# Performance work log

Measured on AMD Instinct MI355X. Metric: run time of the kernel, lower is better.

Reference implementation:

```python
import jax, jax.numpy as jnp
import numpy as np

B, N, D_IN, D_H, D_OUT = 32, 512, 512, 512, 512


def _xavier(key, fan_in, fan_out):
    bound = np.sqrt(6.0 / (fan_in + fan_out))
    return jax.random.uniform(key, (fan_in, fan_out), jnp.float32, -bound, bound)


def setup_inputs() -> dict:
    key = jax.random.key(0)
    ks = jax.random.split(key, 8)
    batch_graph = jax.random.normal(ks[0], (B, N, D_IN), jnp.float32)
    adj = jax.random.uniform(ks[1], (B, N, N), jnp.float32)  # per-graph adjacency blocks
    W0 = _xavier(ks[2], D_IN, D_H)
    b0 = jnp.zeros((D_H,), jnp.float32)
    W1 = _xavier(ks[3], D_H, D_H)
    b1 = jnp.zeros((D_H,), jnp.float32)
    W2 = _xavier(ks[4], D_H, D_OUT)
    b2 = jnp.zeros((D_OUT,), jnp.float32)
    return {"batch_graph": batch_graph, "adj": adj,
            "W0": W0, "b0": b0, "W1": W1, "b1": b1, "W2": W2, "b2": b2}


def _gcn_layer(h, adj, W, b):
    # GraphConvolution: adj @ (h @ W) + b, batched per graph.
    # Equivalent to big_adj @ (big_graph @ W) since big_adj is block-diagonal.
    support = jnp.einsum('bnd,de->bne', h, W)
    return jnp.einsum('bnm,bme->bne', adj, support) + b


def reference(batch_graph, adj, W0, b0, W1, b1, W2, b2):
    # dropout is identity at inference time
    h = jax.nn.relu(_gcn_layer(batch_graph, adj, W0, b0))
    h = jax.nn.relu(_gcn_layer(h, adj, W1, b1))
    h = _gcn_layer(h, adj, W2, b2)  # no activation on final layer
    return h  # [B, N, D_OUT] == torch.stack(big_graph.split(N))
```

## Files before the change

### kernel.cpp

```cpp
#include <hip/hip_runtime.h>
#include <stdint.h>

typedef __bf16 bf16x8 __attribute__((ext_vector_type(8)));
typedef float f32x4 __attribute__((ext_vector_type(4)));
typedef unsigned short u16x4 __attribute__((ext_vector_type(4)));

static __device__ __forceinline__ unsigned short f2bf(float f) {
    union { float f; unsigned u; } v; v.f = f;
    unsigned r = (v.u + 0x7FFFu + ((v.u >> 16) & 1u)) >> 16;
    return (unsigned short)r;
}

__global__ void prep_kernel(const float* __restrict__ X,
                            const float* __restrict__ adj,
                            const float* __restrict__ W0,
                            const float* __restrict__ W1,
                            const float* __restrict__ W2,
                            unsigned short* __restrict__ bufH,
                            unsigned short* __restrict__ adjB,
                            unsigned short* __restrict__ Wt) {
    const int bid = blockIdx.x;
    const int t = threadIdx.x;
    if (bid < 16384) {
        const float* src = (bid < 8192) ? X : adj;
        unsigned short* dst = (bid < 8192) ? bufH : adjB;
        const int i = (bid & 8191) * 256 + t;
        f32x4 v = ((const f32x4*)src)[i];
        u16x4 o;
        o.x = f2bf(v.x); o.y = f2bf(v.y); o.z = f2bf(v.z); o.w = f2bf(v.w);
        ((u16x4*)dst)[i] = o;
    } else {
        const int wb = bid - 16384;
        const int z = wb >> 8;
        const int tile = wb & 255;
        const float* W = (z == 0) ? W0 : (z == 1) ? W1 : W2;
        unsigned short* out = Wt + (size_t)z * (512 * 512);
        __shared__ float tileS[32][33];
        const int bx = (tile & 15) * 32, by = (tile >> 4) * 32;
        const int tx = t & 31, ty = t >> 5;
        #pragma unroll
        for (int r = 0; r < 32; r += 8)
            tileS[ty + r][tx] = W[(size_t)(by + ty + r) * 512 + (bx + tx)];
        __syncthreads();
        #pragma unroll
        for (int r = 0; r < 32; r += 8)
            out[(size_t)(bx + ty + r) * 512 + (by + tx)] = f2bf(tileS[tx][ty + r]);
    }
}

template<int LDA, int LDB, int LDO, bool BIAS, bool RELU, typename OT>
__global__ __launch_bounds__(256, 4)
void gemm_abT_ct(const unsigned short* __restrict__ A,
                 const unsigned short* __restrict__ B,
                 OT* __restrict__ out, const float* __restrict__ bias,
                 long batchA, long batchB, long batchO) {
    __shared__ unsigned short As[128 * 64];
    __shared__ unsigned short Bs[64 * 64];

    const int tid  = threadIdx.x;
    const int lane = tid & 63;
    const int wave = tid >> 6;
    const int quad = lane >> 4;
    const int l16  = lane & 15;
    const int wm   = wave & 1;
    const int wn   = wave >> 1;

    const int m0 = blockIdx.x * 128;
    const int n0 = blockIdx.y * 64;
    A   += (size_t)blockIdx.z * batchA;
    B   += (size_t)blockIdx.z * batchB;
    out += (size_t)blockIdx.z * batchO;

    const int srow = tid >> 3;
    const int spos = (tid & 7) ^ (srow & 7);
    const unsigned short* aG = A + (size_t)(m0 + srow) * LDA + spos * 8;
    const unsigned short* bG = B + (size_t)(n0 + srow) * LDB + spos * 8;
    char* aL = (char*)As + tid * 16;
    char* bL = (char*)Bs + tid * 16;

    f32x4 acc[4][2];
    #pragma unroll
    for (int i = 0; i < 4; ++i)
        #pragma unroll
        for (int j = 0; j < 2; ++j) {
            f32x4 z = {0.f, 0.f, 0.f, 0.f};
            acc[i][j] = z;
        }

    #pragma unroll 1
    for (int kk = 0; kk < 8; ++kk) {
        const int ko = kk * 64;
        #pragma unroll
        for (int r = 0; r < 4; ++r) {
            __builtin_amdgcn_global_load_lds(
                (__attribute__((address_space(1))) void*)(uintptr_t)(aG + (size_t)(r * 32) * LDA + ko),
                (__attribute__((address_space(3))) void*)(aL + r * 4096), 16, 0, 0);
        }
        #pragma unroll
        for (int r = 0; r < 2; ++r) {
            __builtin_amdgcn_global_load_lds(
                (__attribute__((address_space(1))) void*)(uintptr_t)(bG + (size_t)(r * 32) * LDB + ko),
                (__attribute__((address_space(3))) void*)(bL + r * 4096), 16, 0, 0);
        }
        __syncthreads();

        #pragma unroll
        for (int ks = 0; ks < 2; ++ks) {
            bf16x8 af[4], bfr[2];
            #pragma unroll
            for (int i = 0; i < 4; ++i) {
                const int row = wm * 64 + i * 16 + l16;
                const int idx = row * 8 + ((ks * 4 + quad) ^ (row & 7));
                af[i] = *(const bf16x8*)((const char*)As + idx * 16);
            }
            #pragma unroll
            for (int j = 0; j < 2; ++j) {
                const int row = wn * 32 + j * 16 + l16;
                const int idx = row * 8 + ((ks * 4 + quad) ^ (row & 7));
                bfr[j] = *(const bf16x8*)((const char*)Bs + idx * 16);
            }
            #pragma unroll
            for (int i = 0; i < 4; ++i)
                #pragma unroll
                for (int j = 0; j < 2; ++j)
                    acc[i][j] = __builtin_amdgcn_mfma_f32_16x16x32_bf16(af[i], bfr[j], acc[i][j], 0, 0, 0);
        }
        __syncthreads();
    }

    #pragma unroll
    for (int i = 0; i < 4; ++i) {
        const int mb = m0 + wm * 64 + i * 16 + quad * 4;
        f32x4 bb = {0.f, 0.f, 0.f, 0.f};
        if constexpr (BIAS) bb = *(const f32x4*)(bias + mb);
        #pragma unroll
        for (int j = 0; j < 2; ++j) {
            const int n = n0 + wn * 32 + j * 16 + l16;
            f32x4 v = acc[i][j];
            if constexpr (BIAS) v += bb;
            if constexpr (RELU) {
                v.x = v.x > 0.f ? v.x : 0.f;
                v.y = v.y > 0.f ? v.y : 0.f;
                v.z = v.z > 0.f ? v.z : 0.f;
                v.w = v.w > 0.f ? v.w : 0.f;
            }
            if constexpr (sizeof(OT) == 4) {
                *(f32x4*)((float*)out + (size_t)n * LDO + mb) = v;
            } else {
                u16x4 o;
                o.x = f2bf(v.x); o.y = f2bf(v.y); o.z = f2bf(v.z); o.w = f2bf(v.w);
                *(u16x4*)((unsigned short*)out + (size_t)n * LDO + mb) = o;
            }
        }
    }
}

extern "C" void kernel_launch(void* const* d_in, const int* in_sizes, int n_in,
                              void* d_out, int out_size, void* d_ws, size_t ws_size,
                              hipStream_t stream) {
    (void)in_sizes; (void)n_in; (void)out_size; (void)ws_size;
    const float* X   = (const float*)d_in[0];
    const float* adj = (const float*)d_in[1];
    const float* W0  = (const float*)d_in[2];
    const float* b0  = (const float*)d_in[3];
    const float* W1  = (const float*)d_in[4];
    const float* b1  = (const float*)d_in[5];
    const float* W2  = (const float*)d_in[6];
    const float* b2  = (const float*)d_in[7];
    float* out = (float*)d_out;

    char* ws = (char*)d_ws;
    const size_t SZ = 16777216;
    unsigned short* adjB = (unsigned short*)(ws);
    unsigned short* bufH = (unsigned short*)(ws + SZ);
    unsigned short* tmpT = (unsigned short*)(ws + 2 * SZ);
    unsigned short* Wt   = (unsigned short*)(ws + 3 * SZ);
    const unsigned short* W0t = Wt;
    const unsigned short* W1t = Wt + 262144;
    const unsigned short* W2t = Wt + 2 * 262144;

    prep_kernel<<<16384 + 768, 256, 0, stream>>>(X, adj, W0, W1, W2, bufH, adjB, Wt);

    const long BATCH = 512L * 512L;

    gemm_abT_ct<512, 512, 16384, false, false, unsigned short>
        <<<dim3(128, 8, 1), 256, 0, stream>>>(bufH, W0t, tmpT, nullptr, 0, 0, 0);
    gemm_abT_ct<16384, 512, 512, true, true, unsigned short>
        <<<dim3(4, 8, 32), 256, 0, stream>>>(tmpT, adjB, bufH, b0, 512, BATCH, BATCH);
    gemm_abT_ct<512, 512, 16384, false, false, unsigned short>
        <<<dim3(128, 8, 1), 256, 0, stream>>>(bufH, W1t, tmpT, nullptr, 0, 0, 0);
    gemm_abT_ct<16384, 512, 512, true, true, unsigned short>
        <<<dim3(4, 8, 32), 256, 0, stream>>>(tmpT, adjB, bufH, b1, 512, BATCH, BATCH);
    gemm_abT_ct<512, 512, 16384, false, false, unsigned short>
        <<<dim3(128, 8, 1), 256, 0, stream>>>(bufH, W2t, tmpT, nullptr, 0, 0, 0);
    gemm_abT_ct<16384, 512, 512, true, false, float>
        <<<dim3(4, 8, 32), 256, 0, stream>>>(tmpT, adjB, out, b2, 512, BATCH, BATCH);
}
```

Before: 228.5 us.

## Fuse prep and all six GEMMs into one cooperative persistent kernel

Replaces seven separate launches with a single cooperative kernel of 512 blocks that converts inputs, transposes the weights, and runs all six GEMM phases, separated by grid-wide syncs. Each block processes two tiles per phase. The aim is to remove per-launch overhead and tail gaps between kernels. In exchange, occupancy is capped at 2 blocks per CU with fixed tile assignment, grid.sync adds its own cost, and the multi-launch path is kept as a fallback if the cooperative launch fails.

```diff
diff --git a/kernel.cpp b/kernel.cpp
--- a/kernel.cpp
+++ b/kernel.cpp
@@ -1,5 +1,8 @@
 #include <hip/hip_runtime.h>
+#include <hip/hip_cooperative_groups.h>
 #include <stdint.h>
+
+namespace cg = cooperative_groups;
 
 typedef __bf16 bf16x8 __attribute__((ext_vector_type(8)));
 typedef float f32x4 __attribute__((ext_vector_type(4)));
@@ -9,6 +12,208 @@
     union { float f; unsigned u; } v; v.f = f;
     unsigned r = (v.u + 0x7FFFu + ((v.u >> 16) & 1u)) >> 16;
     return (unsigned short)r;
+}
+
+template<bool BIAS, bool RELU, typename OT>
+__device__ __forceinline__
+void gemm_tile(const unsigned short* __restrict__ A, int LDA,
+               const unsigned short* __restrict__ B, int LDB,
+               OT* __restrict__ out, int LDO,
+               const float* __restrict__ bias,
+               int m0, int n0,
+               unsigned short* As, unsigned short* Bs) {
+    const int tid  = threadIdx.x;
+    const int lane = tid & 63;
+    const int wave = tid >> 6;
+    const int quad = lane >> 4;
+    const int l16  = lane & 15;
+    const int wm   = wave & 1;
+    const int wn   = wave >> 1;
+
+    const int srow = tid >> 3;
+    const int spos = (tid & 7) ^ (srow & 7);
+    const unsigned short* aG = A + (size_t)(m0 + srow) * LDA + spos * 8;
+    const unsigned short* bG = B + (size_t)(n0 + srow) * LDB + spos * 8;
+    char* aL = (char*)As + tid * 16;
+    char* bL = (char*)Bs + tid * 16;
+
+    f32x4 acc[4][2];
+    #pragma unroll
+    for (int i = 0; i < 4; ++i)
+        #pragma unroll
+        for (int j = 0; j < 2; ++j) {
+            f32x4 z = {0.f, 0.f, 0.f, 0.f};
+            acc[i][j] = z;
+        }
+
+    #pragma unroll 1
+    for (int kk = 0; kk < 8; ++kk) {
+        const int ko = kk * 64;
+        #pragma unroll
+        for (int r = 0; r < 4; ++r)
+            __builtin_amdgcn_global_load_lds(
+                (__attribute__((address_space(1))) void*)(uintptr_t)(aG + (size_t)(r * 32) * LDA + ko),
+                (__attribute__((address_space(3))) void*)(aL + r * 4096), 16, 0, 0);
+        #pragma unroll
+        for (int r = 0; r < 2; ++r)
+            __builtin_amdgcn_global_load_lds(
+                (__attribute__((address_space(1))) void*)(uintptr_t)(bG + (size_t)(r * 32) * LDB + ko),
+                (__attribute__((address_space(3))) void*)(bL + r * 4096), 16, 0, 0);
+        __syncthreads();
+
+        #pragma unroll
+        for (int ks = 0; ks < 2; ++ks) {
+            bf16x8 af[4], bfr[2];
+            #pragma unroll
+            for (int i = 0; i < 4; ++i) {
+                const int row = wm * 64 + i * 16 + l16;
+                const int idx = row * 8 + ((ks * 4 + quad) ^ (row & 7));
+                af[i] = *(const bf16x8*)((const char*)As + idx * 16);
+            }
+            #pragma unroll
+            for (int j = 0; j < 2; ++j) {
+                const int row = wn * 32 + j * 16 + l16;
+                const int idx = row * 8 + ((ks * 4 + quad) ^ (row & 7));
+                bfr[j] = *(const bf16x8*)((const char*)Bs + idx * 16);
+            }
+            #pragma unroll
+            for (int i = 0; i < 4; ++i)
+                #pragma unroll
+                for (int j = 0; j < 2; ++j)
+                    acc[i][j] = __builtin_amdgcn_mfma_f32_16x16x32_bf16(af[i], bfr[j], acc[i][j], 0, 0, 0);
+        }
+        __syncthreads();
+    }
+
+    #pragma unroll
+    for (int i = 0; i < 4; ++i) {
+        const int mb = m0 + wm * 64 + i * 16 + quad * 4;
+        f32x4 bb = {0.f, 0.f, 0.f, 0.f};
+        if constexpr (BIAS) bb = *(const f32x4*)(bias + (mb - m0) + m0);
+        #pragma unroll
+        for (int j = 0; j < 2; ++j) {
+            const int n = n0 + wn * 32 + j * 16 + l16;
+            f32x4 v = acc[i][j];
+            if constexpr (BIAS) v += bb;
+            if constexpr (RELU) {
+                v.x = v.x > 0.f ? v.x : 0.f;
+                v.y = v.y > 0.f ? v.y : 0.f;
+                v.z = v.z > 0.f ? v.z : 0.f;
+                v.w = v.w > 0.f ? v.w : 0.f;
+            }
+            if constexpr (sizeof(OT) == 4) {
+                *(f32x4*)((float*)out + (size_t)n * LDO + mb) = v;
+            } else {
+                u16x4 o;
+                o.x = f2bf(v.x); o.y = f2bf(v.y); o.z = f2bf(v.z); o.w = f2bf(v.w);
+                *(u16x4*)((unsigned short*)out + (size_t)n * LDO + mb) = o;
+            }
+        }
+    }
+}
+
+__global__ __launch_bounds__(256, 2)
+void fused_gcn(const float* __restrict__ X, const float* __restrict__ adj,
+               const float* __restrict__ W0, const float* __restrict__ b0,
+               const float* __restrict__ W1, const float* __restrict__ b1,
+               const float* __restrict__ W2, const float* __restrict__ b2,
+               float* __restrict__ out,
+               unsigned short* __restrict__ bufH,
+               unsigned short* __restrict__ adjB,
+               unsigned short* __restrict__ tmpT,
+               unsigned short* __restrict__ Wt) {
+    cg::grid_group grid = cg::this_grid();
+    __shared__ unsigned short As[128 * 64];
+    __shared__ unsigned short Bs[64 * 64];
+
+    {
+        const int gt = blockIdx.x * 256 + threadIdx.x;
+        #pragma unroll 1
+        for (int it = 0; it < 16; ++it) {
+            const int i = it * 131072 + gt;
+            f32x4 v = ((const f32x4*)X)[i];
+            u16x4 o;
+            o.x = f2bf(v.x); o.y = f2bf(v.y); o.z = f2bf(v.z); o.w = f2bf(v.w);
+            ((u16x4*)bufH)[i] = o;
+            f32x4 w = ((const f32x4*)adj)[i];
+            u16x4 p;
+            p.x = f2bf(w.x); p.y = f2bf(w.y); p.z = f2bf(w.z); p.w = f2bf(w.w);
+            ((u16x4*)adjB)[i] = p;
+        }
+        float (*tileS)[33] = (float(*)[33])As;
+        const int t = threadIdx.x;
+        const int tx = t & 31, ty = t >> 5;
+        #pragma unroll 1
+        for (int tt = blockIdx.x; tt < 768; tt += 512) {
+            const int z = tt >> 8;
+            const int tile = tt & 255;
+            const float* W = (z == 0) ? W0 : (z == 1) ? W1 : W2;
+            unsigned short* dst = Wt + (size_t)z * (512 * 512);
+            const int bx = (tile & 15) * 32, by = (tile >> 4) * 32;
+            __syncthreads();
+            #pragma unroll
+            for (int r = 0; r < 32; r += 8)
+                tileS[ty + r][tx] = W[(size_t)(by + ty + r) * 512 + (bx + tx)];
+            __syncthreads();
+            #pragma unroll
+            for (int r = 0; r < 32; r += 8)
+                dst[(size_t)(bx + ty + r) * 512 + (by + tx)] = f2bf(tileS[tx][ty + r]);
+        }
+    }
+    grid.sync();
+
+    #pragma unroll 1
+    for (int r = 0; r < 2; ++r) {
+        const int tile = blockIdx.x * 2 + r;
+        gemm_tile<false, false, unsigned short>(bufH, 512, Wt, 512, tmpT, 16384,
+                                                nullptr, (tile >> 3) * 128, (tile & 7) * 64, As, Bs);
+    }
+    grid.sync();
+    #pragma unroll 1
+    for (int r = 0; r < 2; ++r) {
+        const int tile = blockIdx.x * 2 + r;
+        const int z = tile >> 5, mx = (tile >> 3) & 3, nx = tile & 7;
+        gemm_tile<true, true, unsigned short>(tmpT + z * 512, 16384,
+                                              adjB + (size_t)z * 262144, 512,
+                                              bufH + (size_t)z * 262144, 512,
+                                              b0, mx * 128, nx * 64, As, Bs);
+    }
+    grid.sync();
+
+    #pragma unroll 1
+    for (int r = 0; r < 2; ++r) {
+        const int tile = blockIdx.x * 2 + r;
+        gemm_tile<false, false, unsigned short>(bufH, 512, Wt + 262144, 512, tmpT, 16384,
+                                                nullptr, (tile >> 3) * 128, (tile & 7) * 64, As, Bs);
+    }
+    grid.sync();
+    #pragma unroll 1
+    for (int r = 0; r < 2; ++r) {
+        const int tile = blockIdx.x * 2 + r;
+        const int z = tile >> 5, mx = (tile >> 3) & 3, nx = tile & 7;
+        gemm_tile<true, true, unsigned short>(tmpT + z * 512, 16384,
+                                              adjB + (size_t)z * 262144, 512,
+                                              bufH + (size_t)z * 262144, 512,
+                                              b1, mx * 128, nx * 64, As, Bs);
+    }
+    grid.sync();
+
+    #pragma unroll 1
+    for (int r = 0; r < 2; ++r) {
+        const int tile = blockIdx.x * 2 + r;
+        gemm_tile<false, false, unsigned short>(bufH, 512, Wt + 2 * 262144, 512, tmpT, 16384,
+                                                nullptr, (tile >> 3) * 128, (tile & 7) * 64, As, Bs);
+    }
+    grid.sync();
+    #pragma unroll 1
+    for (int r = 0; r < 2; ++r) {
+        const int tile = blockIdx.x * 2 + r;
+        const int z = tile >> 5, mx = (tile >> 3) & 3, nx = tile & 7;
+        gemm_tile<true, false, float>(tmpT + z * 512, 16384,
+                                      adjB + (size_t)z * 262144, 512,
+                                      out + (size_t)z * 262144, 512,
+                                      b2, mx * 128, nx * 64, As, Bs);
+    }
 }
 
 __global__ void prep_kernel(const float* __restrict__ X,
@@ -34,7 +239,7 @@
         const int z = wb >> 8;
         const int tile = wb & 255;
         const float* W = (z == 0) ? W0 : (z == 1) ? W1 : W2;
-        unsigned short* out = Wt + (size_t)z * (512 * 512);
+        unsigned short* dst = Wt + (size_t)z * (512 * 512);
         __shared__ float tileS[32][33];
         const int bx = (tile & 15) * 32, by = (tile >> 4) * 32;
         const int tx = t & 31, ty = t >> 5;
@@ -44,115 +249,22 @@
         __syncthreads();
         #pragma unroll
         for (int r = 0; r < 32; r += 8)
-            out[(size_t)(bx + ty + r) * 512 + (by + tx)] = f2bf(tileS[tx][ty + r]);
+            dst[(size_t)(bx + ty + r) * 512 + (by + tx)] = f2bf(tileS[tx][ty + r]);
     }
 }
 
 template<int LDA, int LDB, int LDO, bool BIAS, bool RELU, typename OT>
-__global__ __launch_bounds__(256, 4)
+__global__ __launch_bounds__(256, 2)
 void gemm_abT_ct(const unsigned short* __restrict__ A,
                  const unsigned short* __restrict__ B,
                  OT* __restrict__ out, const float* __restrict__ bias,
                  long batchA, long batchB, long batchO) {
     __shared__ unsigned short As[128 * 64];
     __shared__ unsigned short Bs[64 * 64];
-
-    const int tid  = threadIdx.x;
-    const int lane = tid & 63;
-    const int wave = tid >> 6;
-    const int quad = lane >> 4;
-    const int l16  = lane & 15;
-    const int wm   = wave & 1;
-    const int wn   = wave >> 1;
-
-    const int m0 = blockIdx.x * 128;
-    const int n0 = blockIdx.y * 64;
-    A   += (size_t)blockIdx.z * batchA;
-    B   += (size_t)blockIdx.z * batchB;
-    out += (size_t)blockIdx.z * batchO;
-
-    const int srow = tid >> 3;
-    const int spos = (tid & 7) ^ (srow & 7);
-    const unsigned short* aG = A + (size_t)(m0 + srow) * LDA + spos * 8;
-    const unsigned short* bG = B + (size_t)(n0 + srow) * LDB + spos * 8;
-    char* aL = (char*)As + tid * 16;
-    char* bL = (char*)Bs + tid * 16;
-
-    f32x4 acc[4][2];
-    #pragma unroll
-    for (int i = 0; i < 4; ++i)
-        #pragma unroll
-        for (int j = 0; j < 2; ++j) {
-            f32x4 z = {0.f, 0.f, 0.f, 0.f};
-            acc[i][j] = z;
-        }
-
-    #pragma unroll 1
-    for (int kk = 0; kk < 8; ++kk) {
-        const int ko = kk * 64;
-        #pragma unroll
-        for (int r = 0; r < 4; ++r) {
-            __builtin_amdgcn_global_load_lds(
-                (__attribute__((address_space(1))) void*)(uintptr_t)(aG + (size_t)(r * 32) * LDA + ko),
-                (__attribute__((address_space(3))) void*)(aL + r * 4096), 16, 0, 0);
-        }
-        #pragma unroll
-        for (int r = 0; r < 2; ++r) {
-            __builtin_amdgcn_global_load_lds(
-                (__attribute__((address_space(1))) void*)(uintptr_t)(bG + (size_t)(r * 32) * LDB + ko),
-                (__attribute__((address_space(3))) void*)(bL + r * 4096), 16, 0, 0);
-        }
-        __syncthreads();
-
-        #pragma unroll
-        for (int ks = 0; ks < 2; ++ks) {
-            bf16x8 af[4], bfr[2];
-            #pragma unroll
-            for (int i = 0; i < 4; ++i) {
-                const int row = wm * 64 + i * 16 + l16;
-                const int idx = row * 8 + ((ks * 4 + quad) ^ (row & 7));
-                af[i] = *(const bf16x8*)((const char*)As + idx * 16);
-            }
-            #pragma unroll
-            for (int j = 0; j < 2; ++j) {
-                const int row = wn * 32 + j * 16 + l16;
-                const int idx = row * 8 + ((ks * 4 + quad) ^ (row & 7));
-                bfr[j] = *(const bf16x8*)((const char*)Bs + idx * 16);
-            }
-            #pragma unroll
-            for (int i = 0; i < 4; ++i)
-                #pragma unroll
-                for (int j = 0; j < 2; ++j)
-                    acc[i][j] = __builtin_amdgcn_mfma_f32_16x16x32_bf16(af[i], bfr[j], acc[i][j], 0, 0, 0);
-        }
-        __syncthreads();
-    }
-
-    #pragma unroll
-    for (int i = 0; i < 4; ++i) {
-        const int mb = m0 + wm * 64 + i * 16 + quad * 4;
-        f32x4 bb = {0.f, 0.f, 0.f, 0.f};
-        if constexpr (BIAS) bb = *(const f32x4*)(bias + mb);
-        #pragma unroll
-        for (int j = 0; j < 2; ++j) {
-            const int n = n0 + wn * 32 + j * 16 + l16;
-            f32x4 v = acc[i][j];
-            if constexpr (BIAS) v += bb;
-            if constexpr (RELU) {
-                v.x = v.x > 0.f ? v.x : 0.f;
-                v.y = v.y > 0.f ? v.y : 0.f;
-                v.z = v.z > 0.f ? v.z : 0.f;
-                v.w = v.w > 0.f ? v.w : 0.f;
-            }
-            if constexpr (sizeof(OT) == 4) {
-                *(f32x4*)((float*)out + (size_t)n * LDO + mb) = v;
-            } else {
-                u16x4 o;
-                o.x = f2bf(v.x); o.y = f2bf(v.y); o.z = f2bf(v.z); o.w = f2bf(v.w);
-                *(u16x4*)((unsigned short*)out + (size_t)n * LDO + mb) = o;
-            }
-        }
-    }
+    gemm_tile<BIAS, RELU, OT>(A + (size_t)blockIdx.z * batchA, LDA,
+                              B + (size_t)blockIdx.z * batchB, LDB,
+                              out + (size_t)blockIdx.z * batchO, LDO,
+                              bias, blockIdx.x * 128, blockIdx.y * 64, As, Bs);
 }
 
 extern "C" void kernel_launch(void* const* d_in, const int* in_sizes, int n_in,
@@ -175,14 +287,19 @@
     unsigned short* bufH = (unsigned short*)(ws + SZ);
     unsigned short* tmpT = (unsigned short*)(ws + 2 * SZ);
     unsigned short* Wt   = (unsigned short*)(ws + 3 * SZ);
+
+    void* args[] = {(void*)&X, (void*)&adj, (void*)&W0, (void*)&b0,
+                    (void*)&W1, (void*)&b1, (void*)&W2, (void*)&b2,
+                    (void*)&out, (void*)&bufH, (void*)&adjB, (void*)&tmpT, (void*)&Wt};
+    hipError_t err = hipLaunchCooperativeKernel((const void*)fused_gcn,
+                                                dim3(512), dim3(256), args, 0, stream);
+    if (err == hipSuccess) return;
+
     const unsigned short* W0t = Wt;
     const unsigned short* W1t = Wt + 262144;
     const unsigned short* W2t = Wt + 2 * 262144;
-
     prep_kernel<<<16384 + 768, 256, 0, stream>>>(X, adj, W0, W1, W2, bufH, adjB, Wt);
-
     const long BATCH = 512L * 512L;
-
     gemm_abT_ct<512, 512, 16384, false, false, unsigned short>
         <<<dim3(128, 8, 1), 256, 0, stream>>>(bufH, W0t, tmpT, nullptr, 0, 0, 0);
     gemm_abT_ct<16384, 512, 512, true, true, unsigned short>
```

New measurement: 660.1 us. 189% more time.

## Double-buffer LDS tiles in GEMM and swizzle block-to-XCD tile mapping

Applied to the files above, without the earlier changes.

Replaces the GEMM kernel with a double-buffered version that issues the next K-slice's global-to-LDS loads before computing the current slice, dropping one barrier per iteration. Blocks are also launched on a flat 1D grid and remapped so that consecutive blocks on the same XCD share A rows or the same graph, which is meant to improve L2 locality. LDS use doubles and launch bounds drop to 3 blocks per CU, which may reduce occupancy.

```diff
diff --git a/kernel.cpp b/kernel.cpp
--- a/kernel.cpp
+++ b/kernel.cpp
@@ -34,7 +34,7 @@
         const int z = wb >> 8;
         const int tile = wb & 255;
         const float* W = (z == 0) ? W0 : (z == 1) ? W1 : W2;
-        unsigned short* out = Wt + (size_t)z * (512 * 512);
+        unsigned short* dst = Wt + (size_t)z * (512 * 512);
         __shared__ float tileS[32][33];
         const int bx = (tile & 15) * 32, by = (tile >> 4) * 32;
         const int tx = t & 31, ty = t >> 5;
@@ -44,19 +44,18 @@
         __syncthreads();
         #pragma unroll
         for (int r = 0; r < 32; r += 8)
-            out[(size_t)(bx + ty + r) * 512 + (by + tx)] = f2bf(tileS[tx][ty + r]);
-    }
-}
-
-template<int LDA, int LDB, int LDO, bool BIAS, bool RELU, typename OT>
-__global__ __launch_bounds__(256, 4)
-void gemm_abT_ct(const unsigned short* __restrict__ A,
-                 const unsigned short* __restrict__ B,
-                 OT* __restrict__ out, const float* __restrict__ bias,
-                 long batchA, long batchB, long batchO) {
-    __shared__ unsigned short As[128 * 64];
-    __shared__ unsigned short Bs[64 * 64];
-
+            dst[(size_t)(bx + ty + r) * 512 + (by + tx)] = f2bf(tileS[tx][ty + r]);
+    }
+}
+
+template<bool BIAS, bool RELU, typename OT>
+__device__ __forceinline__
+void gemm_tile(const unsigned short* __restrict__ A, int LDA,
+               const unsigned short* __restrict__ B, int LDB,
+               OT* __restrict__ out, int LDO,
+               const float* __restrict__ bias,
+               int m0, int n0,
+               unsigned short* As, unsigned short* Bs) {
     const int tid  = threadIdx.x;
     const int lane = tid & 63;
     const int wave = tid >> 6;
@@ -65,18 +64,10 @@
     const int wm   = wave & 1;
     const int wn   = wave >> 1;
 
-    const int m0 = blockIdx.x * 128;
-    const int n0 = blockIdx.y * 64;
-    A   += (size_t)blockIdx.z * batchA;
-    B   += (size_t)blockIdx.z * batchB;
-    out += (size_t)blockIdx.z * batchO;
-
     const int srow = tid >> 3;
     const int spos = (tid & 7) ^ (srow & 7);
     const unsigned short* aG = A + (size_t)(m0 + srow) * LDA + spos * 8;
     const unsigned short* bG = B + (size_t)(n0 + srow) * LDB + spos * 8;
-    char* aL = (char*)As + tid * 16;
-    char* bL = (char*)Bs + tid * 16;
 
     f32x4 acc[4][2];
     #pragma unroll
@@ -87,23 +78,32 @@
             acc[i][j] = z;
         }
 
-    #pragma unroll 1
-    for (int kk = 0; kk < 8; ++kk) {
+    auto issue = [&](int kk, int buf) {
         const int ko = kk * 64;
-        #pragma unroll
-        for (int r = 0; r < 4; ++r) {
+        char* aL = (char*)(As + buf * 8192) + tid * 16;
+        char* bL = (char*)(Bs + buf * 4096) + tid * 16;
+        #pragma unroll
+        for (int r = 0; r < 4; ++r)
             __builtin_amdgcn_global_load_lds(
                 (__attribute__((address_space(1))) void*)(uintptr_t)(aG + (size_t)(r * 32) * LDA + ko),
                 (__attribute__((address_space(3))) void*)(aL + r * 4096), 16, 0, 0);
-        }
-        #pragma unroll
-        for (int r = 0; r < 2; ++r) {
+        #pragma unroll
+        for (int r = 0; r < 2; ++r)
             __builtin_amdgcn_global_load_lds(
                 (__attribute__((address_space(1))) void*)(uintptr_t)(bG + (size_t)(r * 32) * LDB + ko),
                 (__attribute__((address_space(3))) void*)(bL + r * 4096), 16, 0, 0);
-        }
+    };
+
+    issue(0, 0);
+
+    #pragma unroll 1
+    for (int kk = 0; kk < 8; ++kk) {
+        const int cur = kk & 1;
         __syncthreads();
-
+        if (kk < 7) issue(kk + 1, cur ^ 1);
+
+        const unsigned short* Ab = As + cur * 8192;
+        const unsigned short* Bb = Bs + cur * 4096;
         #pragma unroll
         for (int ks = 0; ks < 2; ++ks) {
             bf16x8 af[4], bfr[2];
@@ -111,13 +111,13 @@
             for (int i = 0; i < 4; ++i) {
                 const int row = wm * 64 + i * 16 + l16;
                 const int idx = row * 8 + ((ks * 4 + quad) ^ (row & 7));
-                af[i] = *(const bf16x8*)((const char*)As + idx * 16);
+                af[i] = *(const bf16x8*)((const char*)Ab + idx * 16);
             }
             #pragma unroll
             for (int j = 0; j < 2; ++j) {
                 const int row = wn * 32 + j * 16 + l16;
                 const int idx = row * 8 + ((ks * 4 + quad) ^ (row & 7));
-                bfr[j] = *(const bf16x8*)((const char*)Bs + idx * 16);
+                bfr[j] = *(const bf16x8*)((const char*)Bb + idx * 16);
             }
             #pragma unroll
             for (int i = 0; i < 4; ++i)
@@ -125,7 +125,6 @@
                 for (int j = 0; j < 2; ++j)
                     acc[i][j] = __builtin_amdgcn_mfma_f32_16x16x32_bf16(af[i], bfr[j], acc[i][j], 0, 0, 0);
         }
-        __syncthreads();
     }
 
     #pragma unroll
@@ -152,6 +151,38 @@
                 *(u16x4*)((unsigned short*)out + (size_t)n * LDO + mb) = o;
             }
         }
+    }
+}
+
+__device__ __forceinline__ void feat_tile(int b, int& m0, int& n0) {
+    const int xcd = b & 7, s = b >> 3;
+    m0 = (xcd * 16 + (s >> 3)) * 128;
+    n0 = (s & 7) * 64;
+}
+__device__ __forceinline__ void aggr_tile(int b, int& z, int& m0, int& n0) {
+    const int xcd = b & 7, s = b >> 3;
+    z = xcd + 8 * (s >> 5);
+    const int inner = s & 31;
+    m0 = (inner >> 3) * 128;
+    n0 = (inner & 7) * 64;
+}
+
+template<bool FEAT, bool BIAS, bool RELU, typename OT>
+__global__ __launch_bounds__(256, 3)
+void gemm_swz(const unsigned short* __restrict__ A, int LDA,
+              const unsigned short* __restrict__ B,
+              OT* __restrict__ out, int LDO,
+              const float* __restrict__ bias) {
+    __shared__ unsigned short As[2 * 128 * 64];
+    __shared__ unsigned short Bs[2 * 64 * 64];
+    int z, m0, n0;
+    if constexpr (FEAT) {
+        feat_tile(blockIdx.x, m0, n0);
+        gemm_tile<BIAS, RELU, OT>(A, LDA, B, 512, out, LDO, bias, m0, n0, As, Bs);
+    } else {
+        aggr_tile(blockIdx.x, z, m0, n0);
+        gemm_tile<BIAS, RELU, OT>(A + z * 512, LDA, B + (size_t)z * 262144, 512,
+                                  out + (size_t)z * 262144, LDO, bias, m0, n0, As, Bs);
     }
 }
 
@@ -175,24 +206,19 @@
     unsigned short* bufH = (unsigned short*)(ws + SZ);
     unsigned short* tmpT = (unsigned short*)(ws + 2 * SZ);
     unsigned short* Wt   = (unsigned short*)(ws + 3 * SZ);
-    const unsigned short* W0t = Wt;
-    const unsigned short* W1t = Wt + 262144;
-    const unsigned short* W2t = Wt + 2 * 262144;
 
     prep_kernel<<<16384 + 768, 256, 0, stream>>>(X, adj, W0, W1, W2, bufH, adjB, Wt);
 
-    const long BATCH = 512L * 512L;
-
-    gemm_abT_ct<512, 512, 16384, false, false, unsigned short>
-        <<<dim3(128, 8, 1), 256, 0, stream>>>(bufH, W0t, tmpT, nullptr, 0, 0, 0);
-    gemm_abT_ct<16384, 512, 512, true, true, unsigned short>
-        <<<dim3(4, 8, 32), 256, 0, stream>>>(tmpT, adjB, bufH, b0, 512, BATCH, BATCH);
-    gemm_abT_ct<512, 512, 16384, false, false, unsigned short>
-        <<<dim3(128, 8, 1), 256, 0, stream>>>(bufH, W1t, tmpT, nullptr, 0, 0, 0);
-    gemm_abT_ct<16384, 512, 512, true, true, unsigned short>
-        <<<dim3(4, 8, 32), 256, 0, stream>>>(tmpT, adjB, bufH, b1, 512, BATCH, BATCH);
-    gemm_abT_ct<512, 512, 16384, false, false, unsigned short>
-        <<<dim3(128, 8, 1), 256, 0, stream>>>(bufH, W2t, tmpT, nullptr, 0, 0, 0);
-    gemm_abT_ct<16384, 512, 512, true, false, float>
-        <<<dim3(4, 8, 32), 256, 0, stream>>>(tmpT, adjB, out, b2, 512, BATCH, BATCH);
-}
+    gemm_swz<true, false, false, unsigned short>
+        <<<1024, 256, 0, stream>>>(bufH, 512, Wt, tmpT, 16384, nullptr);
+    gemm_swz<false, true, true, unsigned short>
+        <<<1024, 256, 0, stream>>>(tmpT, 16384, adjB, bufH, 512, b0);
+    gemm_swz<true, false, false, unsigned short>
+        <<<1024, 256, 0, stream>>>(bufH, 512, Wt + 262144, tmpT, 16384, nullptr);
+    gemm_swz<false, true, true, unsigned short>
+        <<<1024, 256, 0, stream>>>(tmpT, 16384, adjB, bufH, 512, b1);
+    gemm_swz<true, false, false, unsigned short>
+        <<<1024, 256, 0, stream>>>(bufH, 512, Wt + 2 * 262144, tmpT, 16384, nullptr);
+    gemm_swz<false, true, false, float>
+        <<<1024, 256, 0, stream>>>(tmpT, 16384, adjB, out, 512, b2);
+}
```

New measurement: 231.5 us. Within noise of the previous version (+1.3%).
